# Performance work log

Hardware: AMD Instinct MI355X
Metric: run time of the kernel (lower is better)

The kernel has to match this reference:

```python
import jax, jax.numpy as jnp
import numpy as np

B, NB, K, C, CM, POS = 8, 1024, 9, 32, 128, 2
SIGMA = 0.5
NEG_SLOPE = 0.01  # nn.LeakyReLU default
BN_EPS = 1e-5


def _leaky(x):
    return jnp.where(x >= 0, x, NEG_SLOPE * x)


def _batchnorm(x, gamma, beta):
    # BatchNorm1d, training-mode batch statistics over the point dimension
    mu = jnp.mean(x, axis=0)
    var = jnp.mean((x - mu) ** 2, axis=0)
    return gamma * (x - mu) * jax.lax.rsqrt(var + BN_EPS) + beta


def setup_inputs() -> dict:
    key = jax.random.key(0)
    ks = jax.random.split(key, 8)
    N = B * NB
    positions = jax.random.normal(ks[0], (N, POS), jnp.float32)
    weights = jax.random.normal(ks[1], (N, C), jnp.float32)
    batch = jnp.full((B,), NB, dtype=jnp.int32)  # uniform point counts per graph
    # KernelConv params: kernel_init='grid' -> 3x3 grid of offsets spanning +-sigma
    g = jnp.linspace(-SIGMA, SIGMA, 3, dtype=jnp.float32)
    kernel_positions = jnp.stack(jnp.meshgrid(g, g, indexing='ij'), axis=-1).reshape(K, POS)
    kernel_weights = (jax.random.normal(ks[2], (K, C, C), jnp.float32) / np.float32(np.sqrt(C * K)))
    conv_norm_gamma = jnp.ones((C,), jnp.float32)
    conv_norm_beta = jnp.zeros((C,), jnp.float32)
    # PyG MLP([C, CM, C+POS], act_first=True, plain_last=True)
    W1 = jax.random.normal(ks[3], (C, CM), jnp.float32) / np.float32(np.sqrt(C))
    b1 = jnp.zeros((CM,), jnp.float32)
    bn_gamma = jnp.ones((CM,), jnp.float32)
    bn_beta = jnp.zeros((CM,), jnp.float32)
    W2 = jax.random.normal(ks[4], (CM, C + POS), jnp.float32) / np.float32(np.sqrt(CM))
    b2 = jnp.zeros((C + POS,), jnp.float32)
    return dict(positions=positions, weights=weights, batch=batch,
                kernel_positions=kernel_positions, kernel_weights=kernel_weights,
                conv_norm_gamma=conv_norm_gamma, conv_norm_beta=conv_norm_beta,
                W1=W1, b1=b1, bn_gamma=bn_gamma, bn_beta=bn_beta, W2=W2, b2=b2)


def reference(positions, weights, batch, kernel_positions, kernel_weights,
              conv_norm_gamma, conv_norm_beta, W1, b1, bn_gamma, bn_beta, W2, b2):
    N = positions.shape[0]
    # --- KernelConv: each point spawns K components at pos + kernel offset ---
    conv_pos = (positions[:, None, :] + kernel_positions[None, :, :])  # [N,K,2]
    conv_w = jnp.einsum('nc,kcd->nkd', weights, kernel_weights)        # [N,K,C]
    conv_pos = conv_pos.reshape(B, NB * K, POS)
    conv_w = conv_w.reshape(B, NB * K, C)
    # --- KernelSample: evaluate Gaussian mixture at original positions ---
    p = positions.reshape(B, NB, POS)
    d2 = (jnp.sum(p * p, -1)[:, :, None]
          + jnp.sum(conv_pos * conv_pos, -1)[:, None, :]
          - 2.0 * jnp.einsum('bnd,bmd->bnm', p, conv_pos))             # [B,NB,NB*K]
    Kmat = jnp.exp(-d2 / (2.0 * SIGMA * SIGMA))
    sampled = jnp.einsum('bnm,bmc->bnc', Kmat, conv_w).reshape(N, C)
    x = _leaky(sampled)                                                 # KernelSample nonlinearity
    # conv_norm + residual add of input weights
    x = _batchnorm(x, conv_norm_gamma, conv_norm_beta) + weights
    # MLP: lin -> act -> batchnorm (act_first) -> plain last lin
    h = _batchnorm(_leaky(x @ W1 + b1), bn_gamma, bn_beta)
    mlp_out = h @ W2 + b2                                               # [N, POS + C]
    delta_pos, delta_w = mlp_out[:, :POS], mlp_out[:, POS:]
    return positions + delta_pos, x + delta_w
```

## Files before the change

kernel.cpp:

```cpp
#include <hip/hip_runtime.h>
#include <hip/hip_bf16.h>

#define BB    8
#define NBB   1024
#define KK    9
#define CC    32
#define CMM   128
#define NTOT  (BB*NBB)
#define MM    (NBB*KK)
#define MS    16
#define MR    (MM/MS)
#define NEG   0.01f
#define EPS   1e-5f
#define L2C   (-2.8853900817779268f)

#define OFF_CWT   0
#define SZ_CWT    (BB*CC*MM/2)
#define OFF_CFX   (OFF_CWT + SZ_CWT)
#define OFF_CFY   (OFF_CFX + BB*MM)
#define OFF_CF0   (OFF_CFY + BB*MM)
#define OFF_PART  (OFF_CF0 + BB*MM)
#define SZ_ONE    (NTOT*CC)
#define SZ_PART   (MS*SZ_ONE)
#define OFF_X0    (OFF_PART)
#define OFF_X     (OFF_PART + SZ_ONE)
#define OFF_H0    (OFF_PART + 2*SZ_ONE)
#define OFF_ST    (OFF_PART + SZ_PART)

typedef __attribute__((ext_vector_type(8))) short short8;
typedef __attribute__((ext_vector_type(4))) float f32x4;
typedef __attribute__((ext_vector_type(2))) float f32x2;

static __device__ __forceinline__ unsigned short f2bf_rne(float f) {
    __hip_bfloat16 h = __float2bfloat16(f);
    return *reinterpret_cast<unsigned short*>(&h);
}

__global__ __launch_bounds__(256) void k_prep(const float* __restrict__ pos,
                                              const float* __restrict__ kpos,
                                              float* __restrict__ cfx,
                                              float* __restrict__ cfy,
                                              float* __restrict__ cf0,
                                              float* __restrict__ stats) {
    int gid = blockIdx.x*256 + threadIdx.x;
    if (blockIdx.x == 0 && threadIdx.x < 320) stats[threadIdx.x] = 0.f;
    if (gid < BB*MM) {
        int b = gid / MM;
        int m = gid - b*MM;
        int np = m / 9, k9 = m - np*9;
        float qx = pos[((size_t)(b*NBB + np))*2 + 0] + kpos[k9*2 + 0];
        float qy = pos[((size_t)(b*NBB + np))*2 + 1] + kpos[k9*2 + 1];
        cfx[gid] = -2.f*L2C*qx;
        cfy[gid] = -2.f*L2C*qy;
        cf0[gid] = L2C*(qx*qx + qy*qy);
    }
}

__global__ __launch_bounds__(256) void k_convw(const float* __restrict__ w,
                                               const float* __restrict__ kw,
                                               short* __restrict__ cwT) {
    __shared__ unsigned short tile[4*32*144];
    int t = threadIdx.x;
    int l = t & 63, wv = t >> 6;
    int lane15 = l & 15, quad = l >> 4;
    int blk = blockIdx.x;
    int b = blk >> 4, nbl = blk & 15;
    int n = b*NBB + nbl*64 + wv*16 + lane15;

    f32x4 w0 = *(const f32x4*)&w[(size_t)n*CC + quad*8];
    f32x4 w1 = *(const f32x4*)&w[(size_t)n*CC + quad*8 + 4];
    union { unsigned short us[8]; short8 s; } bfr;
    bfr.us[0] = f2bf_rne(w0.x); bfr.us[1] = f2bf_rne(w0.y);
    bfr.us[2] = f2bf_rne(w0.z); bfr.us[3] = f2bf_rne(w0.w);
    bfr.us[4] = f2bf_rne(w1.x); bfr.us[5] = f2bf_rne(w1.y);
    bfr.us[6] = f2bf_rne(w1.z); bfr.us[7] = f2bf_rne(w1.w);

    f32x4 acc[KK][2];
    #pragma unroll
    for (int kk = 0; kk < KK; ++kk) {
        #pragma unroll
        for (int ct = 0; ct < 2; ++ct) {
            int c = ct*16 + lane15;
            union { unsigned short us[8]; short8 s; } afr;
            #pragma unroll
            for (int j = 0; j < 8; ++j)
                afr.us[j] = f2bf_rne(kw[(size_t)(kk*CC + quad*8 + j)*CC + c]);
            acc[kk][ct] = __builtin_amdgcn_mfma_f32_16x16x32_bf16(
                afr.s, bfr.s, (f32x4)0.f, 0, 0, 0);
        }
    }
    unsigned short* tw = tile + wv*4608;
    #pragma unroll
    for (int kk = 0; kk < KK; ++kk)
        #pragma unroll
        for (int ct = 0; ct < 2; ++ct)
            #pragma unroll
            for (int reg = 0; reg < 4; ++reg) {
                int c = ct*16 + quad*4 + reg;
                tw[c*144 + lane15*9 + kk] = f2bf_rne(acc[kk][ct][reg]);
            }
    __syncthreads();
    short* dst = cwT + (size_t)b*CC*MM + (size_t)(nbl*64 + wv*16)*9;
    #pragma unroll
    for (int it = 0; it < 9; ++it) {
        int u = it*64 + l;
        int c = u / 18, seg = u - c*18;
        short8 v = *(const short8*)&tw[c*144 + seg*8];
        *(short8*)&dst[(size_t)c*MM + seg*8] = v;
    }
}

__global__ __launch_bounds__(256) void k_sample(const float* __restrict__ pos,
                                                const float* __restrict__ cfx,
                                                const float* __restrict__ cfy,
                                                const float* __restrict__ cf0,
                                                const short* __restrict__ cwT,
                                                float* __restrict__ part) {
    int t = threadIdx.x;
    int l = t & 63, w = t >> 6;
    int blk = blockIdx.x;
    int ks = blk & 15, nb = (blk >> 4) & 7, b = blk >> 7;
    int lane15 = l & 15, quad = l >> 4;
    int nbase = b*NBB + nb*128 + w*32;

    float px[2], py[2], cn[2];
    #pragma unroll
    for (int nt = 0; nt < 2; ++nt) {
        int n = nbase + nt*16 + lane15;
        float x = pos[(size_t)n*2], y = pos[(size_t)n*2 + 1];
        px[nt] = x; py[nt] = y; cn[nt] = L2C*(x*x + y*y);
    }
    f32x4 acc[2][2];
    #pragma unroll
    for (int nt = 0; nt < 2; ++nt) { acc[nt][0] = (f32x4)0.f; acc[nt][1] = (f32x4)0.f; }

    const float* bx = cfx + (size_t)b*MM;
    const float* by = cfy + (size_t)b*MM;
    const float* b0 = cf0 + (size_t)b*MM;
    const short* ca0 = cwT + (size_t)b*CC*MM + (size_t)lane15*MM;
    const short* ca1 = ca0 + (size_t)16*MM;

    int m0 = ks*MR + quad*8;
    #pragma unroll 2
    for (int kk = 0; kk < MR/32; ++kk, m0 += 32) {
        short8 a0 = *(const short8*)&ca0[m0];
        short8 a1 = *(const short8*)&ca1[m0];
        f32x4 vx0 = *(const f32x4*)&bx[m0];
        f32x4 vx1 = *(const f32x4*)&bx[m0 + 4];
        f32x4 vy0 = *(const f32x4*)&by[m0];
        f32x4 vy1 = *(const f32x4*)&by[m0 + 4];
        f32x4 v00 = *(const f32x4*)&b0[m0];
        f32x4 v01 = *(const f32x4*)&b0[m0 + 4];
        #pragma unroll
        for (int nt = 0; nt < 2; ++nt) {
            f32x2 Xv = {px[nt], px[nt]};
            f32x2 Yv = {py[nt], py[nt]};
            f32x2 Cv = {cn[nt], cn[nt]};
            f32x2 t0 = (f32x2){v00.x, v00.y} + Cv;
            t0 = (f32x2){vy0.x, vy0.y}*Yv + t0;
            t0 = (f32x2){vx0.x, vx0.y}*Xv + t0;
            f32x2 t1 = (f32x2){v00.z, v00.w} + Cv;
            t1 = (f32x2){vy0.z, vy0.w}*Yv + t1;
            t1 = (f32x2){vx0.z, vx0.w}*Xv + t1;
            f32x2 t2 = (f32x2){v01.x, v01.y} + Cv;
            t2 = (f32x2){vy1.x, vy1.y}*Yv + t2;
            t2 = (f32x2){vx1.x, vx1.y}*Xv + t2;
            f32x2 t3 = (f32x2){v01.z, v01.w} + Cv;
            t3 = (f32x2){vy1.z, vy1.w}*Yv + t3;
            t3 = (f32x2){vx1.z, vx1.w}*Xv + t3;
            float e0 = __builtin_amdgcn_exp2f(t0.x);
            float e1 = __builtin_amdgcn_exp2f(t0.y);
            float e2 = __builtin_amdgcn_exp2f(t1.x);
            float e3 = __builtin_amdgcn_exp2f(t1.y);
            float e4 = __builtin_amdgcn_exp2f(t2.x);
            float e5 = __builtin_amdgcn_exp2f(t2.y);
            float e6 = __builtin_amdgcn_exp2f(t3.x);
            float e7 = __builtin_amdgcn_exp2f(t3.y);
            union { unsigned int u[4]; short8 s; } bf;
            bf.u[0] = (__float_as_uint(e0) >> 16) | (__float_as_uint(e1) & 0xffff0000u);
            bf.u[1] = (__float_as_uint(e2) >> 16) | (__float_as_uint(e3) & 0xffff0000u);
            bf.u[2] = (__float_as_uint(e4) >> 16) | (__float_as_uint(e5) & 0xffff0000u);
            bf.u[3] = (__float_as_uint(e6) >> 16) | (__float_as_uint(e7) & 0xffff0000u);
            acc[nt][0] = __builtin_amdgcn_mfma_f32_16x16x32_bf16(a0, bf.s, acc[nt][0], 0, 0, 0);
            acc[nt][1] = __builtin_amdgcn_mfma_f32_16x16x32_bf16(a1, bf.s, acc[nt][1], 0, 0, 0);
        }
    }
    #pragma unroll
    for (int nt = 0; nt < 2; ++nt) {
        int n = nbase + nt*16 + lane15;
        #pragma unroll
        for (int ct = 0; ct < 2; ++ct) {
            int c = ct*16 + quad*4;
            *(f32x4*)&part[((size_t)ks*NTOT + n)*CC + c] = acc[nt][ct];
        }
    }
}

__global__ __launch_bounds__(256) void k_leaky_stats(const float* __restrict__ part,
                                                     float* __restrict__ x0,
                                                     float* __restrict__ s1) {
    __shared__ float ss[32], sq[32];
    int t = threadIdx.x;
    if (t < 32) { ss[t] = 0.f; sq[t] = 0.f; }
    __syncthreads();
    float lsum = 0.f, lsq = 0.f;
    int base = blockIdx.x * 1024;
    for (int j = 0; j < 4; ++j) {
        int idx = base + j*256 + t;
        float v = 0.f;
        #pragma unroll
        for (int s = 0; s < MS; ++s) v += part[(size_t)s*SZ_ONE + idx];
        v = v >= 0.f ? v : NEG*v;
        x0[idx] = v;
        lsum += v; lsq = fmaf(v, v, lsq);
    }
    atomicAdd(&ss[t & 31], lsum);
    atomicAdd(&sq[t & 31], lsq);
    __syncthreads();
    if (t < 32) { atomicAdd(&s1[t], ss[t]); atomicAdd(&s1[32+t], sq[t]); }
}

__global__ __launch_bounds__(256) void k_mlp1(const float* __restrict__ x0,
                                              const float* __restrict__ wts,
                                              const float* __restrict__ gma,
                                              const float* __restrict__ bta,
                                              const float* __restrict__ W1,
                                              const float* __restrict__ b1,
                                              const float* __restrict__ s1,
                                              float* __restrict__ x,
                                              float* __restrict__ h0,
                                              float* __restrict__ s2) {
    __shared__ float tile[64*68];
    int t = threadIdx.x;
    int l = t & 63, w = t >> 6;
    int blk = blockIdx.x;
    int nb = blk >> 1, jh = blk & 1;
    int n = nb*64 + l;
    int j0 = jh*64 + w*16;

    float xv[32];
    #pragma unroll
    for (int c = 0; c < 32; ++c) {
        float mu  = s1[c] * (1.f/NTOT);
        float var = s1[32+c]*(1.f/NTOT) - mu*mu;
        float a   = gma[c] * rsqrtf(var + EPS);
        float v   = x0[(size_t)n*CC + c];
        xv[c] = a*(v - mu) + bta[c] + wts[(size_t)n*CC + c];
    }
    if (jh == 0 && w == 0) {
        #pragma unroll
        for (int c = 0; c < 32; c += 4)
            *(float4*)&x[(size_t)n*CC + c] = make_float4(xv[c], xv[c+1], xv[c+2], xv[c+3]);
    }
    float acc[16];
    #pragma unroll
    for (int jj = 0; jj < 16; ++jj) acc[jj] = b1[j0 + jj];
    #pragma unroll 4
    for (int c = 0; c < 32; ++c) {
        float xc = xv[c];
        const float* w1r = W1 + c*CMM + j0;
        #pragma unroll
        for (int jj = 0; jj < 16; ++jj)
            acc[jj] = fmaf(xc, w1r[jj], acc[jj]);
    }
    float* hd = h0 + (size_t)n*CMM + j0;
    #pragma unroll
    for (int jj = 0; jj < 16; ++jj) {
        acc[jj] = acc[jj] >= 0.f ? acc[jj] : NEG*acc[jj];
        tile[(w*16 + jj)*68 + l] = acc[jj];
    }
    #pragma unroll
    for (int jj = 0; jj < 16; jj += 4)
        *(float4*)&hd[jj] = make_float4(acc[jj], acc[jj+1], acc[jj+2], acc[jj+3]);
    __syncthreads();
    int jl = t >> 2, grp = t & 3;
    float lsum = 0.f, lsq = 0.f;
    #pragma unroll
    for (int q = 0; q < 4; ++q) {
        f32x4 v = *(const f32x4*)&tile[jl*68 + grp*16 + q*4];
        lsum += v.x + v.y + v.z + v.w;
        lsq = fmaf(v.x, v.x, fmaf(v.y, v.y, fmaf(v.z, v.z, fmaf(v.w, v.w, lsq))));
    }
    lsum += __shfl_xor(lsum, 1); lsq += __shfl_xor(lsq, 1);
    lsum += __shfl_xor(lsum, 2); lsq += __shfl_xor(lsq, 2);
    if (grp == 0) {
        int jg = jh*64 + jl;
        atomicAdd(&s2[jg], lsum);
        atomicAdd(&s2[CMM + jg], lsq);
    }
}

__global__ __launch_bounds__(256) void k_mlp2(const float* __restrict__ h0,
                                              const float* __restrict__ x,
                                              const float* __restrict__ pos,
                                              const float* __restrict__ g2,
                                              const float* __restrict__ bt2,
                                              const float* __restrict__ W2,
                                              const float* __restrict__ b2,
                                              const float* __restrict__ s2,
                                              float* __restrict__ out) {
    __shared__ float red[4][64][34];
    int t = threadIdx.x;
    int lane = t & 63, w = t >> 6;
    int n = blockIdx.x*64 + lane;
    int j0 = w*32;
    float hv[32];
    #pragma unroll
    for (int q = 0; q < 8; ++q)
        *(float4*)&hv[q*4] = *(const float4*)&h0[(size_t)n*CMM + j0 + q*4];
    #pragma unroll
    for (int jj = 0; jj < 32; ++jj) {
        int j = j0 + jj;
        float mu  = s2[j] * (1.f/NTOT);
        float var = s2[CMM+j]*(1.f/NTOT) - mu*mu;
        float a   = g2[j] * rsqrtf(var + EPS);
        hv[jj] = a*(hv[jj] - mu) + bt2[j];
    }
    float acc[34];
    #pragma unroll
    for (int c = 0; c < 34; ++c) acc[c] = 0.f;
    for (int jj = 0; jj < 32; ++jj) {
        float h = hv[jj];
        const float* w2r = W2 + (size_t)(j0 + jj)*34;
        #pragma unroll
        for (int c = 0; c < 34; ++c)
            acc[c] = fmaf(h, w2r[c], acc[c]);
    }
    #pragma unroll
    for (int c = 0; c < 34; ++c) red[w][lane][c] = acc[c];
    __syncthreads();
    int r = t & 63, seg = t >> 6;
    int c0 = seg*9, c1 = c0 + 9 < 34 ? c0 + 9 : 34;
    int nn = blockIdx.x*64 + r;
    for (int c = c0; c < c1; ++c) {
        float v = red[0][r][c] + red[1][r][c] + red[2][r][c] + red[3][r][c] + b2[c];
        if (c < 2)
            out[(size_t)nn*2 + c] = pos[(size_t)nn*2 + c] + v;
        else
            out[16384 + (size_t)nn*32 + (c-2)] = x[(size_t)nn*32 + (c-2)] + v;
    }
}

extern "C" void kernel_launch(void* const* d_in, const int* in_sizes, int n_in,
                              void* d_out, int out_size, void* d_ws, size_t ws_size,
                              hipStream_t stream) {
    const float* positions = (const float*)d_in[0];
    const float* weights   = (const float*)d_in[1];
    const float* kpos = (const float*)d_in[3];
    const float* kw   = (const float*)d_in[4];
    const float* cg   = (const float*)d_in[5];
    const float* cb   = (const float*)d_in[6];
    const float* W1   = (const float*)d_in[7];
    const float* b1   = (const float*)d_in[8];
    const float* bg   = (const float*)d_in[9];
    const float* bb   = (const float*)d_in[10];
    const float* W2   = (const float*)d_in[11];
    const float* b2   = (const float*)d_in[12];
    float* ws  = (float*)d_ws;
    float* out = (float*)d_out;

    float* s1 = ws + OFF_ST;
    float* s2 = ws + OFF_ST + 64;

    k_prep<<<288, 256, 0, stream>>>(positions, kpos, ws + OFF_CFX, ws + OFF_CFY,
                                    ws + OFF_CF0, s1);
    k_convw<<<128, 256, 0, stream>>>(weights, kw, (short*)(ws + OFF_CWT));
    k_sample<<<1024, 256, 0, stream>>>(positions, ws + OFF_CFX, ws + OFF_CFY,
                                       ws + OFF_CF0, (const short*)(ws + OFF_CWT),
                                       ws + OFF_PART);
    k_leaky_stats<<<256, 256, 0, stream>>>(ws + OFF_PART, ws + OFF_X0, s1);
    k_mlp1<<<256, 256, 0, stream>>>(ws + OFF_X0, weights, cg, cb, W1, b1,
                                    s1, ws + OFF_X, ws + OFF_H0, s2);
    k_mlp2<<<128, 256, 0, stream>>>(ws + OFF_H0, ws + OFF_X, positions,
                                    bg, bb, W2, b2, s2, out);
}
```

Before: 165.9 us.

## Fuse all stages into one cooperative persistent kernel with grid syncs

Replaces six separate kernel launches with a single cooperative kernel that walks through the prep, sample, leaky/stats, MLP1 and MLP2 stages, separated by grid-wide barriers. A multi-launch fallback is kept for when the cooperative launch fails. The MLP stages are also re-tiled to 8 rows per work unit using shared-memory staging, and the conv-weight transpose now writes scattered global stores instead of going through a shared-memory tile. The goal is to remove launch overhead and gaps between stages. The cost is grid-sync latency, lower occupancy from the fused register footprint, and less efficient MLP and transpose access patterns.

Result: slower. 473.6 us (+185.4%).

```diff
diff --git a/kernel.cpp b/kernel.cpp
--- a/kernel.cpp
+++ b/kernel.cpp
@@ -1,5 +1,8 @@
 #include <hip/hip_runtime.h>
 #include <hip/hip_bf16.h>
+#include <hip/hip_cooperative_groups.h>
+
+namespace cg = cooperative_groups;
 
 #define BB    8
 #define NBB   1024
@@ -36,308 +39,263 @@
     return *reinterpret_cast<unsigned short*>(&h);
 }
 
-__global__ __launch_bounds__(256) void k_prep(const float* __restrict__ pos,
-                                              const float* __restrict__ kpos,
-                                              float* __restrict__ cfx,
-                                              float* __restrict__ cfy,
-                                              float* __restrict__ cf0,
-                                              float* __restrict__ stats) {
-    int gid = blockIdx.x*256 + threadIdx.x;
-    if (blockIdx.x == 0 && threadIdx.x < 320) stats[threadIdx.x] = 0.f;
-    if (gid < BB*MM) {
-        int b = gid / MM;
-        int m = gid - b*MM;
-        int np = m / 9, k9 = m - np*9;
-        float qx = pos[((size_t)(b*NBB + np))*2 + 0] + kpos[k9*2 + 0];
-        float qy = pos[((size_t)(b*NBB + np))*2 + 1] + kpos[k9*2 + 1];
-        cfx[gid] = -2.f*L2C*qx;
-        cfy[gid] = -2.f*L2C*qy;
-        cf0[gid] = L2C*(qx*qx + qy*qy);
-    }
-}
-
-__global__ __launch_bounds__(256) void k_convw(const float* __restrict__ w,
-                                               const float* __restrict__ kw,
-                                               short* __restrict__ cwT) {
-    __shared__ unsigned short tile[4*32*144];
+__global__ __launch_bounds__(256, 4) void k_fused(
+        const float* __restrict__ pos,  const float* __restrict__ wts,
+        const float* __restrict__ kpos, const float* __restrict__ kw,
+        const float* __restrict__ cgm,  const float* __restrict__ cbt,
+        const float* __restrict__ W1,   const float* __restrict__ b1,
+        const float* __restrict__ bg,   const float* __restrict__ bb,
+        const float* __restrict__ W2,   const float* __restrict__ b2v,
+        float* __restrict__ ws,         float* __restrict__ out,
+        int mode) {
+    __shared__ __align__(16) float smf[1344];
+
+    short* cwT = (short*)(ws + OFF_CWT);
+    float* cfx = ws + OFF_CFX;
+    float* cfy = ws + OFF_CFY;
+    float* cf0 = ws + OFF_CF0;
+    float* part = ws + OFF_PART;
+    float* x0 = ws + OFF_X0;
+    float* x  = ws + OFF_X;
+    float* h0 = ws + OFF_H0;
+    float* s1 = ws + OFF_ST;
+    float* s2 = ws + OFF_ST + 64;
+
+    int blk = blockIdx.x;
+    int gdim = gridDim.x;
     int t = threadIdx.x;
-    int l = t & 63, wv = t >> 6;
-    int lane15 = l & 15, quad = l >> 4;
-    int blk = blockIdx.x;
-    int b = blk >> 4, nbl = blk & 15;
-    int n = b*NBB + nbl*64 + wv*16 + lane15;
-
-    f32x4 w0 = *(const f32x4*)&w[(size_t)n*CC + quad*8];
-    f32x4 w1 = *(const f32x4*)&w[(size_t)n*CC + quad*8 + 4];
-    union { unsigned short us[8]; short8 s; } bfr;
-    bfr.us[0] = f2bf_rne(w0.x); bfr.us[1] = f2bf_rne(w0.y);
-    bfr.us[2] = f2bf_rne(w0.z); bfr.us[3] = f2bf_rne(w0.w);
-    bfr.us[4] = f2bf_rne(w1.x); bfr.us[5] = f2bf_rne(w1.y);
-    bfr.us[6] = f2bf_rne(w1.z); bfr.us[7] = f2bf_rne(w1.w);
-
-    f32x4 acc[KK][2];
-    #pragma unroll
-    for (int kk = 0; kk < KK; ++kk) {
-        #pragma unroll
-        for (int ct = 0; ct < 2; ++ct) {
-            int c = ct*16 + lane15;
-            union { unsigned short us[8]; short8 s; } afr;
-            #pragma unroll
-            for (int j = 0; j < 8; ++j)
-                afr.us[j] = f2bf_rne(kw[(size_t)(kk*CC + quad*8 + j)*CC + c]);
-            acc[kk][ct] = __builtin_amdgcn_mfma_f32_16x16x32_bf16(
-                afr.s, bfr.s, (f32x4)0.f, 0, 0, 0);
-        }
-    }
-    unsigned short* tw = tile + wv*4608;
-    #pragma unroll
-    for (int kk = 0; kk < KK; ++kk)
-        #pragma unroll
-        for (int ct = 0; ct < 2; ++ct)
-            #pragma unroll
-            for (int reg = 0; reg < 4; ++reg) {
-                int c = ct*16 + quad*4 + reg;
-                tw[c*144 + lane15*9 + kk] = f2bf_rne(acc[kk][ct][reg]);
-            }
-    __syncthreads();
-    short* dst = cwT + (size_t)b*CC*MM + (size_t)(nbl*64 + wv*16)*9;
-    #pragma unroll
-    for (int it = 0; it < 9; ++it) {
-        int u = it*64 + l;
-        int c = u / 18, seg = u - c*18;
-        short8 v = *(const short8*)&tw[c*144 + seg*8];
-        *(short8*)&dst[(size_t)c*MM + seg*8] = v;
-    }
-}
-
-__global__ __launch_bounds__(256) void k_sample(const float* __restrict__ pos,
-                                                const float* __restrict__ cfx,
-                                                const float* __restrict__ cfy,
-                                                const float* __restrict__ cf0,
-                                                const short* __restrict__ cwT,
-                                                float* __restrict__ part) {
-    int t = threadIdx.x;
-    int l = t & 63, w = t >> 6;
-    int blk = blockIdx.x;
-    int ks = blk & 15, nb = (blk >> 4) & 7, b = blk >> 7;
-    int lane15 = l & 15, quad = l >> 4;
-    int nbase = b*NBB + nb*128 + w*32;
-
-    float px[2], py[2], cn[2];
-    #pragma unroll
-    for (int nt = 0; nt < 2; ++nt) {
-        int n = nbase + nt*16 + lane15;
-        float x = pos[(size_t)n*2], y = pos[(size_t)n*2 + 1];
-        px[nt] = x; py[nt] = y; cn[nt] = L2C*(x*x + y*y);
-    }
-    f32x4 acc[2][2];
-    #pragma unroll
-    for (int nt = 0; nt < 2; ++nt) { acc[nt][0] = (f32x4)0.f; acc[nt][1] = (f32x4)0.f; }
-
-    const float* bx = cfx + (size_t)b*MM;
-    const float* by = cfy + (size_t)b*MM;
-    const float* b0 = cf0 + (size_t)b*MM;
-    const short* ca0 = cwT + (size_t)b*CC*MM + (size_t)lane15*MM;
-    const short* ca1 = ca0 + (size_t)16*MM;
-
-    int m0 = ks*MR + quad*8;
-    #pragma unroll 2
-    for (int kk = 0; kk < MR/32; ++kk, m0 += 32) {
-        short8 a0 = *(const short8*)&ca0[m0];
-        short8 a1 = *(const short8*)&ca1[m0];
-        f32x4 vx0 = *(const f32x4*)&bx[m0];
-        f32x4 vx1 = *(const f32x4*)&bx[m0 + 4];
-        f32x4 vy0 = *(const f32x4*)&by[m0];
-        f32x4 vy1 = *(const f32x4*)&by[m0 + 4];
-        f32x4 v00 = *(const f32x4*)&b0[m0];
-        f32x4 v01 = *(const f32x4*)&b0[m0 + 4];
-        #pragma unroll
-        for (int nt = 0; nt < 2; ++nt) {
-            f32x2 Xv = {px[nt], px[nt]};
-            f32x2 Yv = {py[nt], py[nt]};
-            f32x2 Cv = {cn[nt], cn[nt]};
-            f32x2 t0 = (f32x2){v00.x, v00.y} + Cv;
-            t0 = (f32x2){vy0.x, vy0.y}*Yv + t0;
-            t0 = (f32x2){vx0.x, vx0.y}*Xv + t0;
-            f32x2 t1 = (f32x2){v00.z, v00.w} + Cv;
-            t1 = (f32x2){vy0.z, vy0.w}*Yv + t1;
-            t1 = (f32x2){vx0.z, vx0.w}*Xv + t1;
-            f32x2 t2 = (f32x2){v01.x, v01.y} + Cv;
-            t2 = (f32x2){vy1.x, vy1.y}*Yv + t2;
-            t2 = (f32x2){vx1.x, vx1.y}*Xv + t2;
-            f32x2 t3 = (f32x2){v01.z, v01.w} + Cv;
-            t3 = (f32x2){vy1.z, vy1.w}*Yv + t3;
-            t3 = (f32x2){vx1.z, vx1.w}*Xv + t3;
-            float e0 = __builtin_amdgcn_exp2f(t0.x);
-            float e1 = __builtin_amdgcn_exp2f(t0.y);
-            float e2 = __builtin_amdgcn_exp2f(t1.x);
-            float e3 = __builtin_amdgcn_exp2f(t1.y);
-            float e4 = __builtin_amdgcn_exp2f(t2.x);
-            float e5 = __builtin_amdgcn_exp2f(t2.y);
-            float e6 = __builtin_amdgcn_exp2f(t3.x);
-            float e7 = __builtin_amdgcn_exp2f(t3.y);
-            union { unsigned int u[4]; short8 s; } bf;
-            bf.u[0] = (__float_as_uint(e0) >> 16) | (__float_as_uint(e1) & 0xffff0000u);
-            bf.u[1] = (__float_as_uint(e2) >> 16) | (__float_as_uint(e3) & 0xffff0000u);
-            bf.u[2] = (__float_as_uint(e4) >> 16) | (__float_as_uint(e5) & 0xffff0000u);
-            bf.u[3] = (__float_as_uint(e6) >> 16) | (__float_as_uint(e7) & 0xffff0000u);
-            acc[nt][0] = __builtin_amdgcn_mfma_f32_16x16x32_bf16(a0, bf.s, acc[nt][0], 0, 0, 0);
-            acc[nt][1] = __builtin_amdgcn_mfma_f32_16x16x32_bf16(a1, bf.s, acc[nt][1], 0, 0, 0);
-        }
-    }
-    #pragma unroll
-    for (int nt = 0; nt < 2; ++nt) {
-        int n = nbase + nt*16 + lane15;
-        #pragma unroll
-        for (int ct = 0; ct < 2; ++ct) {
-            int c = ct*16 + quad*4;
-            *(f32x4*)&part[((size_t)ks*NTOT + n)*CC + c] = acc[nt][ct];
-        }
-    }
-}
-
-__global__ __launch_bounds__(256) void k_leaky_stats(const float* __restrict__ part,
-                                                     float* __restrict__ x0,
-                                                     float* __restrict__ s1) {
-    __shared__ float ss[32], sq[32];
-    int t = threadIdx.x;
-    if (t < 32) { ss[t] = 0.f; sq[t] = 0.f; }
-    __syncthreads();
-    float lsum = 0.f, lsq = 0.f;
-    int base = blockIdx.x * 1024;
-    for (int j = 0; j < 4; ++j) {
-        int idx = base + j*256 + t;
-        float v = 0.f;
-        #pragma unroll
-        for (int s = 0; s < MS; ++s) v += part[(size_t)s*SZ_ONE + idx];
-        v = v >= 0.f ? v : NEG*v;
-        x0[idx] = v;
-        lsum += v; lsq = fmaf(v, v, lsq);
-    }
-    atomicAdd(&ss[t & 31], lsum);
-    atomicAdd(&sq[t & 31], lsq);
-    __syncthreads();
-    if (t < 32) { atomicAdd(&s1[t], ss[t]); atomicAdd(&s1[32+t], sq[t]); }
-}
-
-__global__ __launch_bounds__(256) void k_mlp1(const float* __restrict__ x0,
-                                              const float* __restrict__ wts,
-                                              const float* __restrict__ gma,
-                                              const float* __restrict__ bta,
-                                              const float* __restrict__ W1,
-                                              const float* __restrict__ b1,
-                                              const float* __restrict__ s1,
-                                              float* __restrict__ x,
-                                              float* __restrict__ h0,
-                                              float* __restrict__ s2) {
-    __shared__ float tile[64*68];
-    int t = threadIdx.x;
-    int l = t & 63, w = t >> 6;
-    int blk = blockIdx.x;
-    int nb = blk >> 1, jh = blk & 1;
-    int n = nb*64 + l;
-    int j0 = jh*64 + w*16;
-
-    float xv[32];
-    #pragma unroll
-    for (int c = 0; c < 32; ++c) {
-        float mu  = s1[c] * (1.f/NTOT);
-        float var = s1[32+c]*(1.f/NTOT) - mu*mu;
-        float a   = gma[c] * rsqrtf(var + EPS);
-        float v   = x0[(size_t)n*CC + c];
-        xv[c] = a*(v - mu) + bta[c] + wts[(size_t)n*CC + c];
-    }
-    if (jh == 0 && w == 0) {
-        #pragma unroll
-        for (int c = 0; c < 32; c += 4)
-            *(float4*)&x[(size_t)n*CC + c] = make_float4(xv[c], xv[c+1], xv[c+2], xv[c+3]);
-    }
-    float acc[16];
-    #pragma unroll
-    for (int jj = 0; jj < 16; ++jj) acc[jj] = b1[j0 + jj];
-    #pragma unroll 4
-    for (int c = 0; c < 32; ++c) {
-        float xc = xv[c];
-        const float* w1r = W1 + c*CMM + j0;
-        #pragma unroll
-        for (int jj = 0; jj < 16; ++jj)
-            acc[jj] = fmaf(xc, w1r[jj], acc[jj]);
-    }
-    float* hd = h0 + (size_t)n*CMM + j0;
-    #pragma unroll
-    for (int jj = 0; jj < 16; ++jj) {
-        acc[jj] = acc[jj] >= 0.f ? acc[jj] : NEG*acc[jj];
-        tile[(w*16 + jj)*68 + l] = acc[jj];
-    }
-    #pragma unroll
-    for (int jj = 0; jj < 16; jj += 4)
-        *(float4*)&hd[jj] = make_float4(acc[jj], acc[jj+1], acc[jj+2], acc[jj+3]);
-    __syncthreads();
-    int jl = t >> 2, grp = t & 3;
-    float lsum = 0.f, lsq = 0.f;
-    #pragma unroll
-    for (int q = 0; q < 4; ++q) {
-        f32x4 v = *(const f32x4*)&tile[jl*68 + grp*16 + q*4];
-        lsum += v.x + v.y + v.z + v.w;
-        lsq = fmaf(v.x, v.x, fmaf(v.y, v.y, fmaf(v.z, v.z, fmaf(v.w, v.w, lsq))));
-    }
-    lsum += __shfl_xor(lsum, 1); lsq += __shfl_xor(lsq, 1);
-    lsum += __shfl_xor(lsum, 2); lsq += __shfl_xor(lsq, 2);
-    if (grp == 0) {
-        int jg = jh*64 + jl;
-        atomicAdd(&s2[jg], lsum);
-        atomicAdd(&s2[CMM + jg], lsq);
-    }
-}
-
-__global__ __launch_bounds__(256) void k_mlp2(const float* __restrict__ h0,
-                                              const float* __restrict__ x,
-                                              const float* __restrict__ pos,
-                                              const float* __restrict__ g2,
-                                              const float* __restrict__ bt2,
-                                              const float* __restrict__ W2,
-                                              const float* __restrict__ b2,
-                                              const float* __restrict__ s2,
-                                              float* __restrict__ out) {
-    __shared__ float red[4][64][34];
-    int t = threadIdx.x;
-    int lane = t & 63, w = t >> 6;
-    int n = blockIdx.x*64 + lane;
-    int j0 = w*32;
-    float hv[32];
-    #pragma unroll
-    for (int q = 0; q < 8; ++q)
-        *(float4*)&hv[q*4] = *(const float4*)&h0[(size_t)n*CMM + j0 + q*4];
-    #pragma unroll
-    for (int jj = 0; jj < 32; ++jj) {
-        int j = j0 + jj;
-        float mu  = s2[j] * (1.f/NTOT);
-        float var = s2[CMM+j]*(1.f/NTOT) - mu*mu;
-        float a   = g2[j] * rsqrtf(var + EPS);
-        hv[jj] = a*(hv[jj] - mu) + bt2[j];
-    }
-    float acc[34];
-    #pragma unroll
-    for (int c = 0; c < 34; ++c) acc[c] = 0.f;
-    for (int jj = 0; jj < 32; ++jj) {
-        float h = hv[jj];
-        const float* w2r = W2 + (size_t)(j0 + jj)*34;
-        #pragma unroll
-        for (int c = 0; c < 34; ++c)
-            acc[c] = fmaf(h, w2r[c], acc[c]);
-    }
-    #pragma unroll
-    for (int c = 0; c < 34; ++c) red[w][lane][c] = acc[c];
-    __syncthreads();
-    int r = t & 63, seg = t >> 6;
-    int c0 = seg*9, c1 = c0 + 9 < 34 ? c0 + 9 : 34;
-    int nn = blockIdx.x*64 + r;
-    for (int c = c0; c < c1; ++c) {
-        float v = red[0][r][c] + red[1][r][c] + red[2][r][c] + red[3][r][c] + b2[c];
-        if (c < 2)
-            out[(size_t)nn*2 + c] = pos[(size_t)nn*2 + c] + v;
-        else
-            out[16384 + (size_t)nn*32 + (c-2)] = x[(size_t)nn*32 + (c-2)] + v;
+
+    if (mode <= 0) {
+        for (int u = blk; u < 417; u += gdim) {
+            if (u < 128) {
+                int l = t & 63, wv = t >> 6;
+                int lane15 = l & 15, quad = l >> 4;
+                int b = u >> 4, nbl = u & 15;
+                int n = b*NBB + nbl*64 + wv*16 + lane15;
+                f32x4 w0 = *(const f32x4*)&wts[(size_t)n*CC + quad*8];
+                f32x4 w1 = *(const f32x4*)&wts[(size_t)n*CC + quad*8 + 4];
+                union { unsigned short us[8]; short8 s; } bfr;
+                bfr.us[0] = f2bf_rne(w0.x); bfr.us[1] = f2bf_rne(w0.y);
+                bfr.us[2] = f2bf_rne(w0.z); bfr.us[3] = f2bf_rne(w0.w);
+                bfr.us[4] = f2bf_rne(w1.x); bfr.us[5] = f2bf_rne(w1.y);
+                bfr.us[6] = f2bf_rne(w1.z); bfr.us[7] = f2bf_rne(w1.w);
+                short* dst = cwT + (size_t)b*CC*MM
+                           + (size_t)(nbl*64 + wv*16 + lane15)*9;
+                for (int kk = 0; kk < KK; ++kk) {
+                    #pragma unroll
+                    for (int ct = 0; ct < 2; ++ct) {
+                        int c = ct*16 + lane15;
+                        union { unsigned short us[8]; short8 s; } afr;
+                        #pragma unroll
+                        for (int j = 0; j < 8; ++j)
+                            afr.us[j] = f2bf_rne(kw[(size_t)(kk*CC + quad*8 + j)*CC + c]);
+                        f32x4 acc = __builtin_amdgcn_mfma_f32_16x16x32_bf16(
+                            afr.s, bfr.s, (f32x4)0.f, 0, 0, 0);
+                        #pragma unroll
+                        for (int reg = 0; reg < 4; ++reg) {
+                            int cr = ct*16 + quad*4 + reg;
+                            dst[(size_t)cr*MM + kk] = (short)f2bf_rne(acc[reg]);
+                        }
+                    }
+                }
+            } else if (u < 416) {
+                int gid = (u - 128)*256 + t;
+                int b = gid / MM;
+                int m = gid - b*MM;
+                int np = m / 9, k9 = m - np*9;
+                float qx = pos[((size_t)(b*NBB + np))*2 + 0] + kpos[k9*2 + 0];
+                float qy = pos[((size_t)(b*NBB + np))*2 + 1] + kpos[k9*2 + 1];
+                cfx[gid] = -2.f*L2C*qx;
+                cfy[gid] = -2.f*L2C*qy;
+                cf0[gid] = L2C*(qx*qx + qy*qy);
+            } else {
+                if (t < 320) s1[t] = 0.f;
+            }
+        }
+    }
+    if (mode < 0) cg::this_grid().sync();
+
+    if (mode < 0 || mode == 1) {
+        int l = t & 63, w = t >> 6;
+        int lane15 = l & 15, quad = l >> 4;
+        for (int u = blk; u < 1024; u += gdim) {
+            int ks = u & 15, nb = (u >> 4) & 7, b = u >> 7;
+            int nbase = b*NBB + nb*128 + w*32;
+
+            float px[2], py[2], cn[2];
+            #pragma unroll
+            for (int nt = 0; nt < 2; ++nt) {
+                int n = nbase + nt*16 + lane15;
+                float X = pos[(size_t)n*2], Y = pos[(size_t)n*2 + 1];
+                px[nt] = X; py[nt] = Y; cn[nt] = L2C*(X*X + Y*Y);
+            }
+            f32x4 acc[2][2];
+            #pragma unroll
+            for (int nt = 0; nt < 2; ++nt) { acc[nt][0] = (f32x4)0.f; acc[nt][1] = (f32x4)0.f; }
+
+            const float* bx = cfx + (size_t)b*MM;
+            const float* by = cfy + (size_t)b*MM;
+            const float* b0 = cf0 + (size_t)b*MM;
+            const short* ca0 = cwT + (size_t)b*CC*MM + (size_t)lane15*MM;
+            const short* ca1 = ca0 + (size_t)16*MM;
+
+            int m0 = ks*MR + quad*8;
+            #pragma unroll 2
+            for (int kk = 0; kk < MR/32; ++kk, m0 += 32) {
+                short8 a0 = *(const short8*)&ca0[m0];
+                short8 a1 = *(const short8*)&ca1[m0];
+                f32x4 vx0 = *(const f32x4*)&bx[m0];
+                f32x4 vx1 = *(const f32x4*)&bx[m0 + 4];
+                f32x4 vy0 = *(const f32x4*)&by[m0];
+                f32x4 vy1 = *(const f32x4*)&by[m0 + 4];
+                f32x4 v00 = *(const f32x4*)&b0[m0];
+                f32x4 v01 = *(const f32x4*)&b0[m0 + 4];
+                #pragma unroll
+                for (int nt = 0; nt < 2; ++nt) {
+                    f32x2 Xv = {px[nt], px[nt]};
+                    f32x2 Yv = {py[nt], py[nt]};
+                    f32x2 Cv = {cn[nt], cn[nt]};
+                    f32x2 t0 = (f32x2){v00.x, v00.y} + Cv;
+                    t0 = (f32x2){vy0.x, vy0.y}*Yv + t0;
+                    t0 = (f32x2){vx0.x, vx0.y}*Xv + t0;
+                    f32x2 t1 = (f32x2){v00.z, v00.w} + Cv;
+                    t1 = (f32x2){vy0.z, vy0.w}*Yv + t1;
+                    t1 = (f32x2){vx0.z, vx0.w}*Xv + t1;
+                    f32x2 t2 = (f32x2){v01.x, v01.y} + Cv;
+                    t2 = (f32x2){vy1.x, vy1.y}*Yv + t2;
+                    t2 = (f32x2){vx1.x, vx1.y}*Xv + t2;
+                    f32x2 t3 = (f32x2){v01.z, v01.w} + Cv;
+                    t3 = (f32x2){vy1.z, vy1.w}*Yv + t3;
+                    t3 = (f32x2){vx1.z, vx1.w}*Xv + t3;
+                    float e0 = __builtin_amdgcn_exp2f(t0.x);
+                    float e1 = __builtin_amdgcn_exp2f(t0.y);
+                    float e2 = __builtin_amdgcn_exp2f(t1.x);
+                    float e3 = __builtin_amdgcn_exp2f(t1.y);
+                    float e4 = __builtin_amdgcn_exp2f(t2.x);
+                    float e5 = __builtin_amdgcn_exp2f(t2.y);
+                    float e6 = __builtin_amdgcn_exp2f(t3.x);
+                    float e7 = __builtin_amdgcn_exp2f(t3.y);
+                    union { unsigned int uu[4]; short8 s; } bf;
+                    bf.uu[0] = (__float_as_uint(e0) >> 16) | (__float_as_uint(e1) & 0xffff0000u);
+                    bf.uu[1] = (__float_as_uint(e2) >> 16) | (__float_as_uint(e3) & 0xffff0000u);
+                    bf.uu[2] = (__float_as_uint(e4) >> 16) | (__float_as_uint(e5) & 0xffff0000u);
+                    bf.uu[3] = (__float_as_uint(e6) >> 16) | (__float_as_uint(e7) & 0xffff0000u);
+                    acc[nt][0] = __builtin_amdgcn_mfma_f32_16x16x32_bf16(a0, bf.s, acc[nt][0], 0, 0, 0);
+                    acc[nt][1] = __builtin_amdgcn_mfma_f32_16x16x32_bf16(a1, bf.s, acc[nt][1], 0, 0, 0);
+                }
+            }
+            #pragma unroll
+            for (int nt = 0; nt < 2; ++nt) {
+                int n = nbase + nt*16 + lane15;
+                #pragma unroll
+                for (int ct = 0; ct < 2; ++ct) {
+                    int c = ct*16 + quad*4;
+                    *(f32x4*)&part[((size_t)ks*NTOT + n)*CC + c] = acc[nt][ct];
+                }
+            }
+        }
+    }
+    if (mode < 0) cg::this_grid().sync();
+
+    if (mode < 0 || mode == 2) {
+        float* red = smf;
+        for (int u = blk; u < 1024; u += gdim) {
+            if (t < 64) red[t] = 0.f;
+            __syncthreads();
+            int idx = u*256 + t;
+            float v = 0.f;
+            #pragma unroll
+            for (int s = 0; s < MS; ++s) v += part[(size_t)s*SZ_ONE + idx];
+            v = v >= 0.f ? v : NEG*v;
+            x0[idx] = v;
+            int c = t & 31;
+            atomicAdd(&red[c], v);
+            atomicAdd(&red[32 + c], v*v);
+            __syncthreads();
+            if (t < 64) atomicAdd(&s1[t], red[t]);
+            __syncthreads();
+        }
+    }
+    if (mode < 0) cg::this_grid().sync();
+
+    if (mode < 0 || mode == 3) {
+        float* xrow = smf;
+        float* st2  = smf + 256;
+        for (int u = blk; u < 1024; u += gdim) {
+            int r = t >> 5, c = t & 31;
+            int n0 = u*8;
+            {
+                int n = n0 + r;
+                float mu  = s1[c] * (1.f/NTOT);
+                float var = s1[32+c]*(1.f/NTOT) - mu*mu;
+                float a   = cgm[c] * rsqrtf(var + EPS);
+                float v   = x0[(size_t)n*CC + c];
+                v = a*(v - mu) + cbt[c] + wts[(size_t)n*CC + c];
+                xrow[r*32 + c] = v;
+                x[(size_t)n*CC + c] = v;
+            }
+            st2[t] = 0.f;
+            __syncthreads();
+            int j = t & 127, rh = t >> 7;
+            float acc4[4];
+            #pragma unroll
+            for (int q = 0; q < 4; ++q) acc4[q] = b1[j];
+            #pragma unroll 4
+            for (int cc2 = 0; cc2 < 32; ++cc2) {
+                float w1c = W1[cc2*CMM + j];
+                #pragma unroll
+                for (int q = 0; q < 4; ++q)
+                    acc4[q] = fmaf(xrow[(rh*4 + q)*32 + cc2], w1c, acc4[q]);
+            }
+            float ls = 0.f, lq = 0.f;
+            #pragma unroll
+            for (int q = 0; q < 4; ++q) {
+                float h = acc4[q] >= 0.f ? acc4[q] : NEG*acc4[q];
+                h0[(size_t)(n0 + rh*4 + q)*CMM + j] = h;
+                ls += h; lq = fmaf(h, h, lq);
+            }
+            atomicAdd(&st2[j], ls);
+            atomicAdd(&st2[128 + j], lq);
+            __syncthreads();
+            atomicAdd(&s2[t], st2[t]);
+            __syncthreads();
+        }
+    }
+    if (mode < 0) cg::this_grid().sync();
+
+    if (mode < 0 || mode == 4) {
+        float* hl   = smf;
+        float* mlpd = smf + 8*132;
+        for (int u = blk; u < 1024; u += gdim) {
+            int n0 = u*8;
+            #pragma unroll
+            for (int i = 0; i < 4; ++i) {
+                int idx = i*256 + t;
+                int j = idx & 127, r = idx >> 7;
+                float v = h0[(size_t)(n0 + r)*CMM + j];
+                float mu  = s2[j] * (1.f/NTOT);
+                float var = s2[CMM+j]*(1.f/NTOT) - mu*mu;
+                float a   = bg[j] * rsqrtf(var + EPS);
+                hl[r*132 + j] = a*(v - mu) + bb[j];
+            }
+            __syncthreads();
+            int r = t >> 5, lane = t & 31;
+            float acc0 = b2v[lane];
+            float acc1 = (lane < 2) ? b2v[32 + lane] : 0.f;
+            for (int j = 0; j < CMM; ++j) {
+                float h = hl[r*132 + j];
+                acc0 = fmaf(h, W2[(size_t)j*34 + lane], acc0);
+                if (lane < 2) acc1 = fmaf(h, W2[(size_t)j*34 + 32 + lane], acc1);
+            }
+            mlpd[r*34 + lane] = acc0;
+            if (lane < 2) mlpd[r*34 + 32 + lane] = acc1;
+            __syncthreads();
+            int n = n0 + r;
+            if (lane < 2)
+                out[(size_t)n*2 + lane] = pos[(size_t)n*2 + lane] + mlpd[r*34 + lane];
+            out[16384 + (size_t)n*32 + lane] = x[(size_t)n*32 + lane] + mlpd[r*34 + 2 + lane];
+            __syncthreads();
+        }
     }
 }
 
@@ -348,8 +306,8 @@
     const float* weights   = (const float*)d_in[1];
     const float* kpos = (const float*)d_in[3];
     const float* kw   = (const float*)d_in[4];
-    const float* cg   = (const float*)d_in[5];
-    const float* cb   = (const float*)d_in[6];
+    const float* cg_  = (const float*)d_in[5];
+    const float* cb_  = (const float*)d_in[6];
     const float* W1   = (const float*)d_in[7];
     const float* b1   = (const float*)d_in[8];
     const float* bg   = (const float*)d_in[9];
@@ -359,18 +317,31 @@
     float* ws  = (float*)d_ws;
     float* out = (float*)d_out;
 
-    float* s1 = ws + OFF_ST;
-    float* s2 = ws + OFF_ST + 64;
-
-    k_prep<<<288, 256, 0, stream>>>(positions, kpos, ws + OFF_CFX, ws + OFF_CFY,
-                                    ws + OFF_CF0, s1);
-    k_convw<<<128, 256, 0, stream>>>(weights, kw, (short*)(ws + OFF_CWT));
-    k_sample<<<1024, 256, 0, stream>>>(positions, ws + OFF_CFX, ws + OFF_CFY,
-                                       ws + OFF_CF0, (const short*)(ws + OFF_CWT),
-                                       ws + OFF_PART);
-    k_leaky_stats<<<256, 256, 0, stream>>>(ws + OFF_PART, ws + OFF_X0, s1);
-    k_mlp1<<<256, 256, 0, stream>>>(ws + OFF_X0, weights, cg, cb, W1, b1,
-                                    s1, ws + OFF_X, ws + OFF_H0, s2);
-    k_mlp2<<<128, 256, 0, stream>>>(ws + OFF_H0, ws + OFF_X, positions,
-                                    bg, bb, W2, b2, s2, out);
+    int nb = 0;
+    int G = 256;
+    if (hipOccupancyMaxActiveBlocksPerMultiprocessor(&nb, k_fused, 256, 0)
+            == hipSuccess && nb > 0) {
+        G = nb * 256;
+        if (G > 1024) G = 1024;
+    }
+
+    int mode = -1;
+    void* args[] = { &positions, &weights, &kpos, &kw, &cg_, &cb_,
+                     &W1, &b1, &bg, &bb, &W2, &b2, &ws, &out, &mode };
+    hipError_t err = hipLaunchCooperativeKernel((const void*)k_fused,
+                                                dim3(G), dim3(256),
+                                                args, 0, stream);
+    if (err != hipSuccess) {
+        (void)hipGetLastError();
+        k_fused<<<417, 256, 0, stream>>>(positions, weights, kpos, kw, cg_, cb_,
+                                         W1, b1, bg, bb, W2, b2, ws, out, 0);
+        k_fused<<<1024, 256, 0, stream>>>(positions, weights, kpos, kw, cg_, cb_,
+                                          W1, b1, bg, bb, W2, b2, ws, out, 1);
+        k_fused<<<1024, 256, 0, stream>>>(positions, weights, kpos, kw, cg_, cb_,
+                                          W1, b1, bg, bb, W2, b2, ws, out, 2);
+        k_fused<<<1024, 256, 0, stream>>>(positions, weights, kpos, kw, cg_, cb_,
+                                          W1, b1, bg, bb, W2, b2, ws, out, 3);
+        k_fused<<<1024, 256, 0, stream>>>(positions, weights, kpos, kw, cg_, cb_,
+                                          W1, b1, bg, bb, W2, b2, ws, out, 4);
+    }
 }
```
